# Performance work log

Hardware: AMD Instinct MI355X
Metric: run time of the kernel (lower is better)

The kernel has to match this reference:

```python
import jax, jax.numpy as jnp
import numpy as np

B, N, IN_DIM, HIDDEN, N_CLASS = 32768, 25, 3, 128, 2

# BODY_25 skeleton edges from the repo
_SRC = np.array([17, 15, 18, 16, 0, 2, 3, 4, 5, 6, 7, 8, 9, 12, 10, 13, 11, 14, 23, 22, 24, 20, 19, 21])
_DST = np.array([15, 0, 16, 0, 1, 1, 2, 3, 1, 5, 6, 1, 8, 8, 9, 12, 10, 13, 22, 11, 11, 19, 14, 14])


def setup_inputs() -> dict:
    key = jax.random.key(0)
    ks = jax.random.split(key, 4)
    # skeleton edges + self loops (dgl.add_self_loop)
    src = jnp.asarray(np.concatenate([_SRC, np.arange(N)]), dtype=jnp.int64)
    dst = jnp.asarray(np.concatenate([_DST, np.arange(N)]), dtype=jnp.int64)
    return {
        "x": jax.random.normal(ks[0], (B, N, IN_DIM), dtype=jnp.float32),
        "src": src,
        "dst": dst,
        "W1": jax.random.normal(ks[1], (IN_DIM, HIDDEN), dtype=jnp.float32) / np.sqrt(IN_DIM),
        "b1": jnp.zeros((HIDDEN,), jnp.float32),
        "W2": jax.random.normal(ks[2], (HIDDEN, HIDDEN), dtype=jnp.float32) / np.sqrt(HIDDEN),
        "b2": jnp.zeros((HIDDEN,), jnp.float32),
        "Wfc": jax.random.normal(ks[3], (HIDDEN, N_CLASS), dtype=jnp.float32) / np.sqrt(HIDDEN),
        "bfc": jnp.zeros((N_CLASS,), jnp.float32),
    }


def reference(x, src, dst, W1, b1, W2, b2, Wfc, bfc):
    # x: [B, N, F] node features for B identical-topology skeleton graphs
    Bn, Nn, _ = x.shape
    ones = jnp.ones(src.shape, x.dtype)
    deg_out = jax.ops.segment_sum(ones, src, num_segments=Nn)  # [N]
    deg_in = jax.ops.segment_sum(ones, dst, num_segments=Nn)   # [N]
    # DGL GraphConv norm='both': D_in^{-1/2} A D_out^{-1/2} X W + b
    cs = jnp.where(deg_out > 0, deg_out ** -0.5, 0.0)
    ci = jnp.where(deg_in > 0, deg_in ** -0.5, 0.0)

    def gconv(h, W, b):
        msg = h[:, src, :] * cs[src][None, :, None]            # gather + src norm
        agg = jnp.zeros_like(h).at[:, dst, :].add(msg)          # scatter-add
        agg = agg * ci[None, :, None]                           # dst norm
        return agg @ W + b

    h = jax.nn.relu(gconv(x, W1, b1))
    h = jax.nn.relu(gconv(h, W2, b2))
    pooled = jnp.mean(h, axis=1)  # dgl.mean_nodes -> [B, HIDDEN]
    return pooled @ Wfc + bfc      # [B, N_CLASS]
```

## Files before the change

kernel.cpp:

```cpp
#include <hip/hip_runtime.h>

#define NN    25
#define FIN   3
#define HID   128
#define GPB   4
#define STRDQ 68

typedef int i32x4 __attribute__((ext_vector_type(4)));
typedef unsigned int uint;

__global__ void w2_absmax(const float* __restrict__ W2, float* __restrict__ scales)
{
    __shared__ float red[256];
    int tid = threadIdx.x;
    float m = 1e-20f;
    for (int i = tid; i < HID * HID; i += 256) m = fmaxf(m, fabsf(W2[i]));
    red[tid] = m;
    __syncthreads();
    for (int s = 128; s > 0; s >>= 1) {
        if (tid < s) red[tid] = fmaxf(red[tid], red[tid + s]);
        __syncthreads();
    }
    if (tid == 0) { scales[0] = red[0]; scales[1] = 32000.0f / red[0]; }
}

static __device__ __forceinline__ long pack8(const int* q)
{
    unsigned long v = 0;
    #pragma unroll
    for (int j = 0; j < 8; ++j)
        v |= ((unsigned long)(unsigned char)(q[j] & 255)) << (8 * j);
    return (long)v;
}

__global__ void pack_w2_i8(const float* __restrict__ W2, const float* __restrict__ scales,
                           long* __restrict__ w2q)
{
    int gi = blockIdx.x * blockDim.x + threadIdx.x;
    if (gi >= 4096) return;
    int l  = gi & 63;
    int nt = (gi >> 6) & 7;
    int kt = (gi >> 9) & 3;
    int p  = gi >> 11;
    int n  = nt * 16 + (l & 15);
    int kb = kt * 32 + (l >> 4) * 8;
    float Sb = scales[1];
    int q8[8];
    #pragma unroll
    for (int j = 0; j < 8; ++j) {
        int qv = (int)rintf(W2[(kb + j) * HID + n] * Sb);
        qv = min(max(qv, -32600), 32600);
        int lo = ((qv + 128) & 255) - 128;
        int hi = (qv - lo) >> 8;
        q8[j] = p ? lo : hi;
    }
    w2q[gi] = pack8(q8);
}

static __device__ __forceinline__ void agg25_inplace(float2* A)
{
    const float cA = 0.40824829f;
    const float cB = 0.31622777f;
    const float cC = 0.44721360f;
    const float cH = 0.5f;
    const float cS = 0.70710678f;
    A[1]  = cB * (A[0] + A[2] + A[5] + A[8]) + cC * A[1];
    A[0]  = cA * (A[15] + A[16] + A[0]);
    A[2]  = cH * (A[3]  + A[2]);
    A[3]  = cH * (A[4]  + A[3]);
    A[4]  = cS *  A[4];
    A[5]  = cH * (A[6]  + A[5]);
    A[6]  = cH * (A[7]  + A[6]);
    A[7]  = cS *  A[7];
    A[8]  = cA * (A[9] + A[12] + A[8]);
    A[9]  = cH * (A[10] + A[9]);
    A[10] = cH * (A[11] + A[10]);
    A[11] = cA * (A[22] + A[24] + A[11]);
    A[12] = cH * (A[13] + A[12]);
    A[13] = cH * (A[14] + A[13]);
    A[14] = cA * (A[19] + A[21] + A[14]);
    A[15] = cH * (A[17] + A[15]);
    A[16] = cH * (A[18] + A[16]);
    A[17] = cS *  A[17];
    A[18] = cS *  A[18];
    A[19] = cH * (A[20] + A[19]);
    A[20] = cS *  A[20];
    A[21] = cS *  A[21];
    A[22] = cH * (A[23] + A[22]);
    A[23] = cS *  A[23];
    A[24] = cS *  A[24];
}

static __device__ __forceinline__ void unpack16(uint4 d, long& hi, long& lo)
{
    uint h01 = __builtin_amdgcn_perm(d.y, d.x, 0x07050301u) ^ 0x80808080u;
    uint h23 = __builtin_amdgcn_perm(d.w, d.z, 0x07050301u) ^ 0x80808080u;
    uint l01 = __builtin_amdgcn_perm(d.y, d.x, 0x06040200u) ^ 0x80808080u;
    uint l23 = __builtin_amdgcn_perm(d.w, d.z, 0x06040200u) ^ 0x80808080u;
    uint hv[2] = {h01, h23};
    uint lv[2] = {l01, l23};
    __builtin_memcpy(&hi, hv, 8);
    __builtin_memcpy(&lo, lv, 8);
}

__global__ __launch_bounds__(256, 5) void gcn_main(
    const float* __restrict__ x,
    const float* __restrict__ W1, const float* __restrict__ b1,
    const float* __restrict__ b2,
    const float* __restrict__ Wfc, const float* __restrict__ bfc,
    const long* __restrict__ w2q, const float* __restrict__ scales,
    float* __restrict__ out)
{
    __shared__ __align__(16) uint  bufQ[GPB][NN][STRDQ];
    __shared__ __align__(16) float xs[GPB][80];
    __shared__ float s_b2[HID];
    __shared__ float s_wfc[HID * 2];
    __shared__ float s_bfc[2];

    const int tid  = threadIdx.x;
    const int w    = tid >> 6;
    const int lane = tid & 63;
    const int g    = blockIdx.x * GPB + w;
    const int c0   = lane * 2;
    const int m0   = lane & 15;
    const int quad = lane >> 4;

    if (tid < HID) s_b2[tid] = b2[tid];
    s_wfc[tid] = Wfc[tid];
    if (tid < 2) s_bfc[tid] = bfc[tid];
    __syncthreads();

    const float Sb = scales[1];
    float msk1[4];
    #pragma unroll
    for (int rr = 0; rr < 4; ++rr)
        msk1[rr] = (quad * 4 + rr < 9) ? 1.0f : 0.0f;

    const float* xg = x + (size_t)g * (NN * FIN);
    xs[w][lane] = xg[lane];
    if (lane < NN * FIN - 64) xs[w][64 + lane] = xg[64 + lane];
    asm volatile("s_waitcnt lgkmcnt(0)" ::: "memory");

    float2 w1r0 = *(const float2*)(W1 + 0 * HID + c0);
    float2 w1r1 = *(const float2*)(W1 + 1 * HID + c0);
    float2 w1r2 = *(const float2*)(W1 + 2 * HID + c0);
    float2 A[NN];
    const float4* xv = (const float4*)&xs[w][0];
    #pragma unroll
    for (int grp = 0; grp < 6; ++grp) {
        float4 p = xv[grp * 3 + 0];
        float4 q = xv[grp * 3 + 1];
        float4 r = xv[grp * 3 + 2];
        float xa[4][3] = {{p.x, p.y, p.z}, {p.w, q.x, q.y},
                          {q.z, q.w, r.x}, {r.y, r.z, r.w}};
        #pragma unroll
        for (int j = 0; j < 4; ++j) {
            int n = grp * 4 + j;
            A[n].x = fmaf(xa[j][0], w1r0.x, fmaf(xa[j][1], w1r1.x, xa[j][2] * w1r2.x));
            A[n].y = fmaf(xa[j][0], w1r0.y, fmaf(xa[j][1], w1r1.y, xa[j][2] * w1r2.y));
        }
    }
    {
        float x0 = xs[w][72], x1 = xs[w][73], x2 = xs[w][74];
        A[24].x = fmaf(x0, w1r0.x, fmaf(x1, w1r1.x, x2 * w1r2.x));
        A[24].y = fmaf(x0, w1r0.y, fmaf(x1, w1r1.y, x2 * w1r2.y));
    }

    float2 b1v = *(const float2*)(b1 + c0);
    agg25_inplace(A);
    #pragma unroll
    for (int n = 0; n < NN; ++n) {
        A[n].x = fmaxf(A[n].x + b1v.x, 0.0f);
        A[n].y = fmaxf(A[n].y + b1v.y, 0.0f);
    }

    agg25_inplace(A);

    float am = 1e-20f;
    #pragma unroll
    for (int n = 0; n < NN; ++n)
        am = fmaxf(am, fmaxf(fabsf(A[n].x), fabsf(A[n].y)));
    #pragma unroll
    for (int off = 32; off > 0; off >>= 1)
        am = fmaxf(am, __shfl_xor(am, off));
    const float Sa = 32000.0f / am;

    #pragma unroll
    for (int n = 0; n < NN; ++n) {
        uint qx = (uint)fmaf(A[n].x, Sa, 32896.5f);
        uint qy = (uint)fmaf(A[n].y, Sa, 32896.5f);
        bufQ[w][n][lane] = __builtin_amdgcn_perm(qy, qx, 0x05040100u);
    }
    asm volatile("s_waitcnt lgkmcnt(0)" ::: "memory");

    const int m1  = min(16 + m0, NN - 1);
    const int kq4 = quad * 4;

    long ah[2][4], al[2][4];
    #pragma unroll
    for (int kt = 0; kt < 4; ++kt) {
        uint4 d0 = *(const uint4*)&bufQ[w][m0][kt * 16 + kq4];
        uint4 d1 = *(const uint4*)&bufQ[w][m1][kt * 16 + kq4];
        unpack16(d0, ah[0][kt], al[0][kt]);
        unpack16(d1, ah[1][kt], al[1][kt]);
    }

    const float rsL = 256.0f / (Sa * Sb);

    float s0 = 0.0f, s1 = 0.0f;
    #pragma unroll
    for (int nt = 0; nt < 8; ++nt) {
        i32x4 aHH[2], aX[2];
        #pragma unroll
        for (int mt = 0; mt < 2; ++mt) { aHH[mt] = (i32x4)0; aX[mt] = (i32x4)0; }

        #pragma unroll
        for (int kt = 0; kt < 4; ++kt) {
            long bh = w2q[(size_t)(((0 + kt) * 8 + nt) * 64 + lane)];
            long bl = w2q[(size_t)(((4 + kt) * 8 + nt) * 64 + lane)];
            aHH[0] = __builtin_amdgcn_mfma_i32_16x16x32_i8(ah[0][kt], bh, aHH[0], 0, 0, 0);
            aHH[1] = __builtin_amdgcn_mfma_i32_16x16x32_i8(ah[1][kt], bh, aHH[1], 0, 0, 0);
            aX[0]  = __builtin_amdgcn_mfma_i32_16x16x32_i8(ah[0][kt], bl, aX[0], 0, 0, 0);
            aX[0]  = __builtin_amdgcn_mfma_i32_16x16x32_i8(al[0][kt], bh, aX[0], 0, 0, 0);
            aX[1]  = __builtin_amdgcn_mfma_i32_16x16x32_i8(ah[1][kt], bl, aX[1], 0, 0, 0);
            aX[1]  = __builtin_amdgcn_mfma_i32_16x16x32_i8(al[1][kt], bh, aX[1], 0, 0, 0);
        }

        float b2c = s_b2[nt * 16 + m0];
        float2 wfc = *(const float2*)&s_wfc[(nt * 16 + m0) * 2];
        float s = 0.0f;
        #pragma unroll
        for (int rr = 0; rr < 4; ++rr) {
            int ci = (int)(((uint)aHH[0][rr] << 8)) + aX[0][rr];
            s += fmaxf(fmaf((float)ci, rsL, b2c), 0.0f);
        }
        #pragma unroll
        for (int rr = 0; rr < 4; ++rr) {
            int ci = (int)(((uint)aHH[1][rr] << 8)) + aX[1][rr];
            float hv = fmaxf(fmaf((float)ci, rsL, b2c), 0.0f);
            s = fmaf(hv, msk1[rr], s);
        }
        s0 = fmaf(s, wfc.x, s0);
        s1 = fmaf(s, wfc.y, s1);
    }

    #pragma unroll
    for (int off = 32; off > 0; off >>= 1) {
        s0 += __shfl_down(s0, off);
        s1 += __shfl_down(s1, off);
    }
    if (lane == 0) {
        out[g * 2 + 0] = s0 * (1.0f / 25.0f) + s_bfc[0];
        out[g * 2 + 1] = s1 * (1.0f / 25.0f) + s_bfc[1];
    }
}

extern "C" void kernel_launch(void* const* d_in, const int* in_sizes, int n_in,
                              void* d_out, int out_size, void* d_ws, size_t ws_size,
                              hipStream_t stream)
{
    const float* x   = (const float*)d_in[0];
    const float* W1  = (const float*)d_in[3];
    const float* b1  = (const float*)d_in[4];
    const float* W2  = (const float*)d_in[5];
    const float* b2  = (const float*)d_in[6];
    const float* Wfc = (const float*)d_in[7];
    const float* bfc = (const float*)d_in[8];
    float* out = (float*)d_out;

    const int Btot = in_sizes[0] / (NN * FIN);

    float* scales = (float*)d_ws;
    long*  w2q    = (long*)((char*)d_ws + 256);

    hipLaunchKernelGGL(w2_absmax, dim3(1), dim3(256), 0, stream, W2, scales);
    hipLaunchKernelGGL(pack_w2_i8, dim3(16), dim3(256), 0, stream, W2, scales, w2q);
    hipLaunchKernelGGL(gcn_main, dim3(Btot / GPB), dim3(256), 0, stream,
                       x, W1, b1, b2, Wfc, bfc, w2q, scales, out);
}
```

Before: 174.9 us.

## Shrink LDS footprint with XOR-swizzled buffer and raise occupancy target to six blocks

Replaces the padded LDS stride of 68 with an unpadded 64-wide buffer that uses an XOR swizzle to avoid bank conflicts. The x staging area now reuses the quantized buffer, and b2 and bfc are read into registers instead of LDS. Together these cut shared memory per block, and the launch bound goes from 5 to 6 blocks per CU so more waves can be resident. The risks are register pressure from the tighter launch bound and the extra b2 registers, and a possible bank-conflict pattern from the new swizzle.

Result: slower. 273.5 us (+56.4%).

```diff
diff --git a/kernel.cpp b/kernel.cpp
--- a/kernel.cpp
+++ b/kernel.cpp
@@ -4,7 +4,6 @@
 #define FIN   3
 #define HID   128
 #define GPB   4
-#define STRDQ 68
 
 typedef int i32x4 __attribute__((ext_vector_type(4)));
 typedef unsigned int uint;
@@ -103,7 +102,7 @@
     __builtin_memcpy(&lo, lv, 8);
 }
 
-__global__ __launch_bounds__(256, 5) void gcn_main(
+__global__ __launch_bounds__(256, 6) void gcn_main(
     const float* __restrict__ x,
     const float* __restrict__ W1, const float* __restrict__ b1,
     const float* __restrict__ b2,
@@ -111,11 +110,8 @@
     const long* __restrict__ w2q, const float* __restrict__ scales,
     float* __restrict__ out)
 {
-    __shared__ __align__(16) uint  bufQ[GPB][NN][STRDQ];
-    __shared__ __align__(16) float xs[GPB][80];
-    __shared__ float s_b2[HID];
+    __shared__ __align__(16) uint bufQ[GPB][NN][64];
     __shared__ float s_wfc[HID * 2];
-    __shared__ float s_bfc[2];
 
     const int tid  = threadIdx.x;
     const int w    = tid >> 6;
@@ -125,34 +121,40 @@
     const int m0   = lane & 15;
     const int quad = lane >> 4;
 
-    if (tid < HID) s_b2[tid] = b2[tid];
     s_wfc[tid] = Wfc[tid];
-    if (tid < 2) s_bfc[tid] = bfc[tid];
     __syncthreads();
 
-    const float Sb = scales[1];
+    float b2v[8];
+    #pragma unroll
+    for (int nt = 0; nt < 8; ++nt) b2v[nt] = b2[nt * 16 + m0];
+    const float  Sb   = scales[1];
+    const float2 bfcv = *(const float2*)bfc;
     float msk1[4];
     #pragma unroll
     for (int rr = 0; rr < 4; ++rr)
         msk1[rr] = (quad * 4 + rr < 9) ? 1.0f : 0.0f;
 
+    uint* xsw = &bufQ[w][0][0];
     const float* xg = x + (size_t)g * (NN * FIN);
-    xs[w][lane] = xg[lane];
-    if (lane < NN * FIN - 64) xs[w][64 + lane] = xg[64 + lane];
+    xsw[lane] = __float_as_uint(xg[lane]);
+    if (lane < NN * FIN - 64) xsw[64 + lane] = __float_as_uint(xg[64 + lane]);
     asm volatile("s_waitcnt lgkmcnt(0)" ::: "memory");
 
     float2 w1r0 = *(const float2*)(W1 + 0 * HID + c0);
     float2 w1r1 = *(const float2*)(W1 + 1 * HID + c0);
     float2 w1r2 = *(const float2*)(W1 + 2 * HID + c0);
     float2 A[NN];
-    const float4* xv = (const float4*)&xs[w][0];
+    const uint4* xv = (const uint4*)xsw;
     #pragma unroll
     for (int grp = 0; grp < 6; ++grp) {
-        float4 p = xv[grp * 3 + 0];
-        float4 q = xv[grp * 3 + 1];
-        float4 r = xv[grp * 3 + 2];
-        float xa[4][3] = {{p.x, p.y, p.z}, {p.w, q.x, q.y},
-                          {q.z, q.w, r.x}, {r.y, r.z, r.w}};
+        uint4 pu = xv[grp * 3 + 0];
+        uint4 qu = xv[grp * 3 + 1];
+        uint4 ru = xv[grp * 3 + 2];
+        float xa[4][3] = {
+            {__uint_as_float(pu.x), __uint_as_float(pu.y), __uint_as_float(pu.z)},
+            {__uint_as_float(pu.w), __uint_as_float(qu.x), __uint_as_float(qu.y)},
+            {__uint_as_float(qu.z), __uint_as_float(qu.w), __uint_as_float(ru.x)},
+            {__uint_as_float(ru.y), __uint_as_float(ru.z), __uint_as_float(ru.w)}};
         #pragma unroll
         for (int j = 0; j < 4; ++j) {
             int n = grp * 4 + j;
@@ -161,7 +163,9 @@
         }
     }
     {
-        float x0 = xs[w][72], x1 = xs[w][73], x2 = xs[w][74];
+        float x0 = __uint_as_float(xsw[72]);
+        float x1 = __uint_as_float(xsw[73]);
+        float x2 = __uint_as_float(xsw[74]);
         A[24].x = fmaf(x0, w1r0.x, fmaf(x1, w1r1.x, x2 * w1r2.x));
         A[24].y = fmaf(x0, w1r0.y, fmaf(x1, w1r1.y, x2 * w1r2.y));
     }
@@ -189,18 +193,20 @@
     for (int n = 0; n < NN; ++n) {
         uint qx = (uint)fmaf(A[n].x, Sa, 32896.5f);
         uint qy = (uint)fmaf(A[n].y, Sa, 32896.5f);
-        bufQ[w][n][lane] = __builtin_amdgcn_perm(qy, qx, 0x05040100u);
+        bufQ[w][n][lane ^ ((n & 7) * 4)] = __builtin_amdgcn_perm(qy, qx, 0x05040100u);
     }
     asm volatile("s_waitcnt lgkmcnt(0)" ::: "memory");
 
     const int m1  = min(16 + m0, NN - 1);
     const int kq4 = quad * 4;
+    const int sw0 = (m0 & 7) * 4;
+    const int sw1 = (m1 & 7) * 4;
 
     long ah[2][4], al[2][4];
     #pragma unroll
     for (int kt = 0; kt < 4; ++kt) {
-        uint4 d0 = *(const uint4*)&bufQ[w][m0][kt * 16 + kq4];
-        uint4 d1 = *(const uint4*)&bufQ[w][m1][kt * 16 + kq4];
+        uint4 d0 = *(const uint4*)&bufQ[w][m0][(kt * 16 + kq4) ^ sw0];
+        uint4 d1 = *(const uint4*)&bufQ[w][m1][(kt * 16 + kq4) ^ sw1];
         unpack16(d0, ah[0][kt], al[0][kt]);
         unpack16(d1, ah[1][kt], al[1][kt]);
     }
@@ -226,7 +232,7 @@
             aX[1]  = __builtin_amdgcn_mfma_i32_16x16x32_i8(al[1][kt], bh, aX[1], 0, 0, 0);
         }
 
-        float b2c = s_b2[nt * 16 + m0];
+        float b2c = b2v[nt];
         float2 wfc = *(const float2*)&s_wfc[(nt * 16 + m0) * 2];
         float s = 0.0f;
         #pragma unroll
@@ -250,8 +256,8 @@
         s1 += __shfl_down(s1, off);
     }
     if (lane == 0) {
-        out[g * 2 + 0] = s0 * (1.0f / 25.0f) + s_bfc[0];
-        out[g * 2 + 1] = s1 * (1.0f / 25.0f) + s_bfc[1];
+        out[g * 2 + 0] = s0 * (1.0f / 25.0f) + bfcv.x;
+        out[g * 2 + 1] = s1 * (1.0f / 25.0f) + bfcv.y;
     }
 }
 
```
